# Performance work log

Measured on AMD Instinct MI355X. Metric: run time of the kernel, lower is better.

## Reference

```python
import jax, jax.numpy as jnp
import numpy as np

B = 4
N_TOTAL = 40000
N_SRC0, N_DST0, E0 = 30000, 15000, 360000
N_DST1, E1 = 7500, 180000
D_IN, OUT = 64, 32
H1, C1 = 8, 8
H2, C2 = 1, OUT
NEG_SLOPE = 0.2


def setup_inputs() -> dict:
    key = jax.random.key(0)
    ks = jax.random.split(key, 16)
    inp = {
        'x': jax.random.normal(ks[0], (B, N_TOTAL, D_IN), dtype=jnp.float32),
        'n_id0': jax.random.randint(ks[1], (N_SRC0,), 0, N_SRC0),
        'res_n_id0': jax.random.randint(ks[2], (N_DST0,), 0, N_SRC0),
        'edge_src0': jax.random.randint(ks[3], (E0,), 0, N_SRC0),
        'edge_dst0': jax.random.randint(ks[4], (E0,), 0, N_DST0),
        'res_n_id1': jax.random.randint(ks[5], (N_DST1,), 0, N_DST0),
        'edge_src1': jax.random.randint(ks[6], (E1,), 0, N_DST0),
        'edge_dst1': jax.random.randint(ks[7], (E1,), 0, N_DST1),
        # GATConv params (Glorot-ish scale)
        'W1': jax.random.normal(ks[8], (D_IN, H1 * C1), dtype=jnp.float32) / np.sqrt(D_IN),
        'att_src1': jax.random.normal(ks[9], (H1, C1), dtype=jnp.float32) / np.sqrt(C1),
        'att_dst1': jax.random.normal(ks[10], (H1, C1), dtype=jnp.float32) / np.sqrt(C1),
        'b1': jnp.zeros((H1 * C1,), dtype=jnp.float32),
        'W2': jax.random.normal(ks[11], (H1 * C1, H2 * C2), dtype=jnp.float32) / np.sqrt(H1 * C1),
        'att_src2': jax.random.normal(ks[12], (H2, C2), dtype=jnp.float32) / np.sqrt(C2),
        'att_dst2': jax.random.normal(ks[13], (H2, C2), dtype=jnp.float32) / np.sqrt(C2),
        'b2': jnp.zeros((H2 * C2,), dtype=jnp.float32),
    }
    return inp


def gat_conv(x_src, x_dst, src, dst, W, a_src, a_dst, bias, n_dst, H, C):
    """Bipartite PyG-style GATConv (concat=True, eval mode, no self-loops)."""
    b = x_src.shape[0]
    hs = (x_src @ W).reshape(b, -1, H, C)            # [B, Ns, H, C]
    hd = (x_dst @ W).reshape(b, -1, H, C)            # [B, Nd, H, C]
    es = jnp.einsum('bnhc,hc->bnh', hs, a_src)       # [B, Ns, H]
    ed = jnp.einsum('bnhc,hc->bnh', hd, a_dst)       # [B, Nd, H]
    e = jax.nn.leaky_relu(es[:, src] + ed[:, dst], NEG_SLOPE)  # [B, E, H]
    eT = jnp.swapaxes(e, 0, 1)                       # [E, B, H] (segment over axis 0)
    m = jax.ops.segment_max(eT, dst, num_segments=n_dst)
    p = jnp.exp(eT - m[dst])
    den = jax.ops.segment_sum(p, dst, num_segments=n_dst)
    alpha = p / den[dst]                             # [E, B, H]
    msg = alpha[..., None] * jnp.swapaxes(hs[:, src], 0, 1)    # [E, B, H, C]
    out = jax.ops.segment_sum(msg, dst, num_segments=n_dst)    # [Nd, B, H, C]
    out = jnp.swapaxes(out, 0, 1).reshape(b, n_dst, H * C)
    return out + bias


def reference(x, n_id0, res_n_id0, edge_src0, edge_dst0, res_n_id1, edge_src1,
              edge_dst1, W1, att_src1, att_dst1, b1, W2, att_src2, att_dst2, b2):
    xt = x[:, n_id0, :]                                        # [B, N_SRC0, D_IN]
    h = gat_conv(xt, xt[:, res_n_id0, :], edge_src0, edge_dst0,
                 W1, att_src1, att_dst1, b1, N_DST0, H1, C1)
    h = jax.nn.elu(h)                                          # dropout = identity (eval)
    out = gat_conv(h, h[:, res_n_id1, :], edge_src1, edge_dst1,
                   W2, att_src2, att_dst2, b2, N_DST1, H2, C2)
    return out                                                 # [B, N_DST1, OUT]
```

## Files before the change

### kernel.cpp

```cpp
#include <hip/hip_runtime.h>

#define NB 4
#define NT 40000
#define NS0 30000
#define ND0 15000
#define NE0 360000
#define ND1 7500
#define NE1 180000
#define NEG 0.2f

#define CAP 64
#define K1B ((NB*NS0)/64)
#define SB8 ((NE0 + NE1 + 2047)/2048)

#define BKT(p) ((((p) & 7) << 3) | ((p) >> 3))

typedef __attribute__((ext_vector_type(8))) short bf8;
typedef __attribute__((ext_vector_type(4))) float f4;
typedef __attribute__((ext_vector_type(2))) float f2;

__device__ __forceinline__ unsigned short f2bf(float f) {
    unsigned u = __float_as_uint(f);
    u += 0x7FFF + ((u >> 16) & 1);
    return (unsigned short)(u >> 16);
}
__device__ __forceinline__ f2 upk(unsigned u) {
    f2 r;
    r.x = __uint_as_float(u << 16);
    r.y = __uint_as_float(u & 0xFFFF0000u);
    return r;
}

__global__ __launch_bounds__(256) void kA_gemm_scat(
        const float* __restrict__ x, const int* __restrict__ n_id0,
        const float* __restrict__ W1, const float* __restrict__ a_src,
        const float* __restrict__ a_dst,
        unsigned short* __restrict__ ht1b, float* __restrict__ es1, float* __restrict__ ed1,
        const int* __restrict__ esrc0, const int* __restrict__ edst0,
        const int* __restrict__ esrc1, const int* __restrict__ edst1,
        int* __restrict__ cur0, int* __restrict__ cur1,
        int* __restrict__ srcsort0, int* __restrict__ srcsort1) {
    __shared__ unsigned short xtb[64*72];
    __shared__ unsigned short wtb[64*72];
    __shared__ float asl[64], adl[64];
    if (blockIdx.x >= K1B) {
        int base = (blockIdx.x - K1B) * 2048 + threadIdx.x;
        #pragma unroll
        for (int p = 0; p < 8; ++p) {
            int t = base + p * 256;
            if (t < NE0) {
                int d = edst0[t];
                int pos = atomicAdd(&cur0[d], 1);
                if (pos < CAP) srcsort0[d*CAP + BKT(pos)] = esrc0[t];
            } else if (t < NE0 + NE1) {
                int e = t - NE0;
                int d = edst1[e];
                int pos = atomicAdd(&cur1[d], 1);
                if (pos < CAP) srcsort1[d*CAP + BKT(pos)] = esrc1[e];
            }
        }
        return;
    }
    int bid = blockIdx.x;
    int t = threadIdx.x;
    {
        int k = t >> 2, nb = (t & 3) * 16;
        const float* wrow = &W1[k*64 + nb];
        #pragma unroll
        for (int j = 0; j < 16; j += 4) {
            float4 v = *(const float4*)&wrow[j];
            wtb[(nb+j+0)*72 + k] = f2bf(v.x);
            wtb[(nb+j+1)*72 + k] = f2bf(v.y);
            wtb[(nb+j+2)*72 + k] = f2bf(v.z);
            wtb[(nb+j+3)*72 + k] = f2bf(v.w);
        }
    }
    if (t < 64) { asl[t] = a_src[t]; adl[t] = a_dst[t]; }
    {
        int r   = t >> 2;
        int sub = t & 3;
        int row_s = bid * 64 + r;
        int bs = row_s / NS0;
        int ns = row_s - bs * NS0;
        const float* xrow = x + ((size_t)(bs * NT + n_id0[ns])) * 64;
        #pragma unroll
        for (int j = 0; j < 4; ++j) {
            int kf = (sub + j*4) * 4;
            float4 v = *(const float4*)&xrow[kf];
            ushort4 u;
            u.x = f2bf(v.x); u.y = f2bf(v.y); u.z = f2bf(v.z); u.w = f2bf(v.w);
            *(ushort4*)&xtb[r*72 + kf] = u;
        }
    }
    __syncthreads();
    int w = t >> 6, lane = t & 63, quad = lane >> 4, cl = lane & 15;
    int arow = 16*w + cl;
    bf8 a0 = *(const bf8*)&xtb[arow*72 + quad*8];
    bf8 a1 = *(const bf8*)&xtb[arow*72 + 32 + quad*8];
    f4 acc[4];
    #pragma unroll
    for (int sub = 0; sub < 4; ++sub) {
        int n = sub*16 + cl;
        bf8 b0 = *(const bf8*)&wtb[n*72 + quad*8];
        bf8 b1v = *(const bf8*)&wtb[n*72 + 32 + quad*8];
        f4 c = {0.f, 0.f, 0.f, 0.f};
        c = __builtin_amdgcn_mfma_f32_16x16x32_bf16(a0, b0, c, 0, 0, 0);
        c = __builtin_amdgcn_mfma_f32_16x16x32_bf16(a1, b1v, c, 0, 0, 0);
        acc[sub] = c;
    }
    __syncthreads();
    unsigned short* ob = xtb;
    #pragma unroll
    for (int sub = 0; sub < 4; ++sub)
        #pragma unroll
        for (int r = 0; r < 4; ++r)
            ob[(16*w + 4*quad + r)*64 + sub*16 + cl] = f2bf(acc[sub][r]);
    int rbase = bid*64 + 16*w + quad*4;
    #pragma unroll
    for (int r = 0; r < 4; ++r) {
        #pragma unroll
        for (int sub = 0; sub < 4; ++sub) {
            int col = sub*16 + cl;
            float ps = acc[sub][r] * asl[col];
            float pd = acc[sub][r] * adl[col];
            ps += __shfl_xor(ps, 1); ps += __shfl_xor(ps, 2); ps += __shfl_xor(ps, 4);
            pd += __shfl_xor(pd, 1); pd += __shfl_xor(pd, 2); pd += __shfl_xor(pd, 4);
            if ((cl & 7) == 0) {
                int h = sub*2 + (cl >> 3);
                es1[(rbase + r)*8 + h] = ps;
                ed1[(rbase + r)*8 + h] = pd;
            }
        }
    }
    __syncthreads();
    {
        int row = t >> 3;
        int c8  = t & 7;
        #pragma unroll
        for (int rep = 0; rep < 2; ++rep) {
            int rr2 = row + rep*32;
            uint4 v = *(const uint4*)&ob[rr2*64 + c8*8];
            *(uint4*)&ht1b[((size_t)(bid*64 + rr2))*64 + c8*8] = v;
        }
    }
}

__global__ __launch_bounds__(256) void k3_agg1_node2(
        const int* __restrict__ srcsort0, const int* __restrict__ cur0,
        const int* __restrict__ res0,
        const float* __restrict__ es1, const float* __restrict__ ed1,
        const unsigned short* __restrict__ ht1b, const float* __restrict__ b1,
        const float* __restrict__ W2, const float* __restrict__ a_src2,
        const float* __restrict__ a_dst2,
        float* __restrict__ ht2, float* __restrict__ es2, float* __restrict__ ed2) {
    __shared__ float W2t[32][68];
    __shared__ float as2[32], ad2[32];
    __shared__ float b1l[64];
    __shared__ float hsh[4][64];
    int t = threadIdx.x;
    {
        float4 v0 = *(const float4*)&W2[t*8];
        float4 v1 = *(const float4*)&W2[t*8 + 4];
        int k = t >> 2, c = (t & 3) * 8;
        W2t[c+0][k] = v0.x; W2t[c+1][k] = v0.y; W2t[c+2][k] = v0.z; W2t[c+3][k] = v0.w;
        W2t[c+4][k] = v1.x; W2t[c+5][k] = v1.y; W2t[c+6][k] = v1.z; W2t[c+7][k] = v1.w;
    }
    if (t < 32) { as2[t] = a_src2[t]; ad2[t] = a_dst2[t]; }
    if (t < 64) b1l[t] = b1[t];
    __syncthreads();
    int xcd = blockIdx.x & 7;
    int b = xcd >> 1;
    int chunk = (blockIdx.x >> 3) * 2 + (xcd & 1);
    int wv = t >> 6;
    int d = chunk * 4 + wv;
    int lane = t & 63;
    int grp = lane >> 3;
    int c = lane & 7;
    int dn = res0[d];
    float edv = ed1[(b*NS0 + dn)*8 + c];
    int start = d * CAP;
    int cnt = min(cur0[d], CAP);
    const float* esb = es1 + (size_t)b*NS0*8;
    const unsigned short* htb = ht1b + (size_t)b*NS0*64;
    f2 a01 = {0.f, 0.f}, a23 = {0.f, 0.f}, a45 = {0.f, 0.f}, a67 = {0.f, 0.f};
    float wsum = 0.f;
    int i = grp;
    int pp = start + grp*8;
    int4 sv = *(const int4*)&srcsort0[pp];
    bool v0 = i      < cnt, v1 = i + 8  < cnt,
         v2 = i + 16 < cnt, v3 = i + 24 < cnt;
    int s0 = v0 ? sv.x : 0;
    int s1 = v1 ? sv.y : 0;
    int s2 = v2 ? sv.z : 0;
    int s3 = v3 ? sv.w : 0;
    for (;;) {
        float e0 = esb[s0*8 + c], e1 = esb[s1*8 + c];
        float e2 = esb[s2*8 + c], e3 = esb[s3*8 + c];
        uint4 h0 = *(const uint4*)&htb[(size_t)s0*64 + c*8];
        uint4 h1 = *(const uint4*)&htb[(size_t)s1*64 + c*8];
        uint4 h2 = *(const uint4*)&htb[(size_t)s2*64 + c*8];
        uint4 h3 = *(const uint4*)&htb[(size_t)s3*64 + c*8];
        int ni = i + 32;
        bool nv0 = false, nv1 = false, nv2 = false, nv3 = false;
        int t0 = 0, t1 = 0, t2 = 0, t3 = 0;
        if (ni < cnt) {
            int4 nsv = *(const int4*)&srcsort0[pp + 4];
            nv0 = true;            nv1 = ni + 8  < cnt;
            nv2 = ni + 16 < cnt;   nv3 = ni + 24 < cnt;
            t0 =       nsv.x;
            t1 = nv1 ? nsv.y : 0;
            t2 = nv2 ? nsv.z : 0;
            t3 = nv3 ? nsv.w : 0;
        }
        e0 += edv; e1 += edv; e2 += edv; e3 += edv;
        e0 = e0 > 0.f ? e0 : NEG * e0;
        e1 = e1 > 0.f ? e1 : NEG * e1;
        e2 = e2 > 0.f ? e2 : NEG * e2;
        e3 = e3 > 0.f ? e3 : NEG * e3;
        float w0 = v0 ? __expf(e0) : 0.f;
        float w1 = v1 ? __expf(e1) : 0.f;
        float w2 = v2 ? __expf(e2) : 0.f;
        float w3 = v3 ? __expf(e3) : 0.f;
        a01 += w0 * upk(h0.x); a23 += w0 * upk(h0.y);
        a45 += w0 * upk(h0.z); a67 += w0 * upk(h0.w);
        a01 += w1 * upk(h1.x); a23 += w1 * upk(h1.y);
        a45 += w1 * upk(h1.z); a67 += w1 * upk(h1.w);
        a01 += w2 * upk(h2.x); a23 += w2 * upk(h2.y);
        a45 += w2 * upk(h2.z); a67 += w2 * upk(h2.w);
        a01 += w3 * upk(h3.x); a23 += w3 * upk(h3.y);
        a45 += w3 * upk(h3.z); a67 += w3 * upk(h3.w);
        wsum += (w0 + w1) + (w2 + w3);
        i = ni; pp += 4;
        s0 = t0; s1 = t1; s2 = t2; s3 = t3;
        v0 = nv0; v1 = nv1; v2 = nv2; v3 = nv3;
        if (i >= cnt) break;
    }
    float acc[8] = {a01.x, a01.y, a23.x, a23.y, a45.x, a45.y, a67.x, a67.y};
    int g0 = grp & 1, g1 = (grp >> 1) & 1, g2 = grp >> 2;
    float n0, n1, n2, n3;
    {
        float s, r;
        s = g0 ? acc[0] : acc[1]; r = __shfl_xor(s, 8);  n0 = (g0 ? acc[1] : acc[0]) + r;
        s = g0 ? acc[2] : acc[3]; r = __shfl_xor(s, 8);  n1 = (g0 ? acc[3] : acc[2]) + r;
        s = g0 ? acc[4] : acc[5]; r = __shfl_xor(s, 8);  n2 = (g0 ? acc[5] : acc[4]) + r;
        s = g0 ? acc[6] : acc[7]; r = __shfl_xor(s, 8);  n3 = (g0 ? acc[7] : acc[6]) + r;
    }
    float m0, m1;
    {
        float s, r;
        s = g1 ? n0 : n1; r = __shfl_xor(s, 16); m0 = (g1 ? n1 : n0) + r;
        s = g1 ? n2 : n3; r = __shfl_xor(s, 16); m1 = (g1 ? n3 : n2) + r;
    }
    float fin;
    {
        float s = g2 ? m0 : m1; float r = __shfl_xor(s, 32); fin = (g2 ? m1 : m0) + r;
    }
    wsum += __shfl_xor(wsum, 8); wsum += __shfl_xor(wsum, 16); wsum += __shfl_xor(wsum, 32);
    float inv = cnt > 0 ? 1.f / wsum : 0.f;
    float o = fin * inv + b1l[(c << 3) | grp];
    o = o > 0.f ? o : __expf(o) - 1.f;
    hsh[wv][(c << 3) | grp] = o;
    int c2 = lane & 31, half = lane >> 5;
    const float4* hp = (const float4*)&hsh[wv][half * 32];
    const float4* wp = (const float4*)&W2t[c2][half * 32];
    float acc2 = 0.f;
    #pragma unroll
    for (int q = 0; q < 8; ++q) {
        float4 hv = hp[q];
        float4 w4 = wp[q];
        acc2 = fmaf(hv.x, w4.x, acc2); acc2 = fmaf(hv.y, w4.y, acc2);
        acc2 = fmaf(hv.z, w4.z, acc2); acc2 = fmaf(hv.w, w4.w, acc2);
    }
    acc2 += __shfl_xor(acc2, 32);
    float ps = acc2 * as2[c2];
    float pd = acc2 * ad2[c2];
    ps += __shfl_xor(ps, 1); ps += __shfl_xor(ps, 2); ps += __shfl_xor(ps, 4);
    ps += __shfl_xor(ps, 8); ps += __shfl_xor(ps, 16);
    pd += __shfl_xor(pd, 1); pd += __shfl_xor(pd, 2); pd += __shfl_xor(pd, 4);
    pd += __shfl_xor(pd, 8); pd += __shfl_xor(pd, 16);
    int row = b*ND0 + d;
    if (half == 0) ht2[(size_t)row*32 + c2] = acc2;
    if (lane == 0) { es2[row] = ps; ed2[row] = pd; }
}

__global__ __launch_bounds__(256) void k7_agg2(
        const int* __restrict__ srcsort1, const int* __restrict__ cur1,
        const int* __restrict__ res1,
        const float* __restrict__ es2, const float* __restrict__ ed2,
        const float* __restrict__ ht2, const float* __restrict__ b2,
        float* __restrict__ outp) {
    int xcd = blockIdx.x & 7;
    int b = xcd >> 1;
    int chunk = (blockIdx.x >> 3) * 2 + (xcd & 1);
    if (chunk >= ND1/4) return;
    int d = chunk * 4 + (threadIdx.x >> 6);
    int lane = threadIdx.x & 63;
    int grp = lane >> 3;
    int c = lane & 7;
    int dn = res1[d];
    float edv = ed2[b*ND0 + dn];
    int start = d * CAP;
    int cnt = min(cur1[d], CAP);
    const float* esb = es2 + (size_t)b*ND0;
    const float* htb = ht2 + (size_t)b*ND0*32;
    f4 accv = {0.f, 0.f, 0.f, 0.f};
    float wsum = 0.f;
    int i = grp;
    int pp = start + grp*8;
    int4 sv = *(const int4*)&srcsort1[pp];
    bool v0 = i      < cnt, v1 = i + 8  < cnt,
         v2 = i + 16 < cnt, v3 = i + 24 < cnt;
    int s0 = v0 ? sv.x : 0;
    int s1 = v1 ? sv.y : 0;
    int s2 = v2 ? sv.z : 0;
    int s3 = v3 ? sv.w : 0;
    for (;;) {
        float lg0 = esb[s0], lg1 = esb[s1], lg2 = esb[s2], lg3 = esb[s3];
        f4 h0 = *(const f4*)&htb[(size_t)s0*32 + c*4];
        f4 h1 = *(const f4*)&htb[(size_t)s1*32 + c*4];
        f4 h2 = *(const f4*)&htb[(size_t)s2*32 + c*4];
        f4 h3 = *(const f4*)&htb[(size_t)s3*32 + c*4];
        int ni = i + 32;
        bool nv0 = false, nv1 = false, nv2 = false, nv3 = false;
        int t0 = 0, t1 = 0, t2 = 0, t3 = 0;
        if (ni < cnt) {
            int4 nsv = *(const int4*)&srcsort1[pp + 4];
            nv0 = true;            nv1 = ni + 8  < cnt;
            nv2 = ni + 16 < cnt;   nv3 = ni + 24 < cnt;
            t0 =       nsv.x;
            t1 = nv1 ? nsv.y : 0;
            t2 = nv2 ? nsv.z : 0;
            t3 = nv3 ? nsv.w : 0;
        }
        lg0 += edv; lg1 += edv; lg2 += edv; lg3 += edv;
        lg0 = lg0 > 0.f ? lg0 : NEG * lg0;
        lg1 = lg1 > 0.f ? lg1 : NEG * lg1;
        lg2 = lg2 > 0.f ? lg2 : NEG * lg2;
        lg3 = lg3 > 0.f ? lg3 : NEG * lg3;
        float w0 = v0 ? __expf(lg0) : 0.f;
        float w1 = v1 ? __expf(lg1) : 0.f;
        float w2 = v2 ? __expf(lg2) : 0.f;
        float w3 = v3 ? __expf(lg3) : 0.f;
        accv += w0 * h0;
        accv += w1 * h1;
        accv += w2 * h2;
        accv += w3 * h3;
        wsum += (w0 + w1) + (w2 + w3);
        i = ni; pp += 4;
        s0 = t0; s1 = t1; s2 = t2; s3 = t3;
        v0 = nv0; v1 = nv1; v2 = nv2; v3 = nv3;
        if (i >= cnt) break;
    }
    float ax = accv.x, ay = accv.y, az = accv.z, aw = accv.w;
    ax += __shfl_xor(ax, 8); ax += __shfl_xor(ax, 16); ax += __shfl_xor(ax, 32);
    ay += __shfl_xor(ay, 8); ay += __shfl_xor(ay, 16); ay += __shfl_xor(ay, 32);
    az += __shfl_xor(az, 8); az += __shfl_xor(az, 16); az += __shfl_xor(az, 32);
    aw += __shfl_xor(aw, 8); aw += __shfl_xor(aw, 16); aw += __shfl_xor(aw, 32);
    wsum += __shfl_xor(wsum, 8); wsum += __shfl_xor(wsum, 16); wsum += __shfl_xor(wsum, 32);
    if (grp == 0) {
        float inv = cnt > 0 ? 1.f / wsum : 0.f;
        float4 bb = *(const float4*)&b2[c*4];
        float4 o;
        o.x = ax*inv + bb.x; o.y = ay*inv + bb.y;
        o.z = az*inv + bb.z; o.w = aw*inv + bb.w;
        *(float4*)&outp[((size_t)(b*ND1 + d))*32 + c*4] = o;
    }
}

extern "C" void kernel_launch(void* const* d_in, const int* in_sizes, int n_in,
                              void* d_out, int out_size, void* d_ws, size_t ws_size,
                              hipStream_t stream) {
    const float* x        = (const float*)d_in[0];
    const int*   n_id0    = (const int*)d_in[1];
    const int*   res0     = (const int*)d_in[2];
    const int*   esrc0    = (const int*)d_in[3];
    const int*   edst0    = (const int*)d_in[4];
    const int*   res1     = (const int*)d_in[5];
    const int*   esrc1    = (const int*)d_in[6];
    const int*   edst1    = (const int*)d_in[7];
    const float* W1       = (const float*)d_in[8];
    const float* a_src1   = (const float*)d_in[9];
    const float* a_dst1   = (const float*)d_in[10];
    const float* b1       = (const float*)d_in[11];
    const float* W2       = (const float*)d_in[12];
    const float* a_src2   = (const float*)d_in[13];
    const float* a_dst2   = (const float*)d_in[14];
    const float* b2       = (const float*)d_in[15];
    float* outp = (float*)d_out;

    char* base = (char*)d_ws;
    unsigned short* ht1b = (unsigned short*)base;
    float* es1  = (float*)(base + 15360000);
    float* ed1  = es1 + 960000;
    float* ht2  = ed1 + 960000;
    float* es2  = ht2 + 1920000;
    float* ed2  = es2 + 60000;
    int* cur0     = (int*)(ed2 + 60000);
    int* cur1     = cur0 + ND0;
    int* srcsort0 = cur1 + ND1;
    int* srcsort1 = srcsort0 + ND0*CAP;

    hipMemsetAsync(cur0, 0, (ND0 + ND1) * sizeof(int), stream);
    kA_gemm_scat<<<K1B + SB8, 256, 0, stream>>>(x, n_id0, W1, a_src1, a_dst1,
                                                ht1b, es1, ed1,
                                                esrc0, edst0, esrc1, edst1,
                                                cur0, cur1, srcsort0, srcsort1);
    k3_agg1_node2<<<NB*(ND0/4), 256, 0, stream>>>(srcsort0, cur0, res0, es1, ed1, ht1b, b1,
                                                  W2, a_src2, a_dst2, ht2, es2, ed2);
    k7_agg2<<<7504, 256, 0, stream>>>(srcsort1, cur1, res1, es2, ed2, ht2, b2, outp);
}
```

Before: 184.1 us.

## Interleave scatter blocks with GEMM blocks and process two row tiles per block

```diff
diff --git a/kernel.cpp b/kernel.cpp
--- a/kernel.cpp
+++ b/kernel.cpp
@@ -10,8 +10,8 @@
 #define NEG 0.2f
 
 #define CAP 64
-#define K1B ((NB*NS0)/64)
-#define SB8 ((NE0 + NE1 + 2047)/2048)
+#define GEMB 938
+#define SBI  264
 
 #define BKT(p) ((((p) & 7) << 3) | ((p) >> 3))
 
@@ -43,8 +43,16 @@
     __shared__ unsigned short xtb[64*72];
     __shared__ unsigned short wtb[64*72];
     __shared__ float asl[64], adl[64];
-    if (blockIdx.x >= K1B) {
-        int base = (blockIdx.x - K1B) * 2048 + threadIdx.x;
+    int bid = blockIdx.x;
+    int sid = -1, gid = 0;
+    if (bid < SBI*4) {
+        if ((bid & 3) == 0) sid = bid >> 2;
+        else gid = (bid >> 2) * 3 + (bid & 3) - 1;
+    } else {
+        gid = bid - SBI;
+    }
+    if (sid >= 0) {
+        int base = sid * 2048 + threadIdx.x;
         #pragma unroll
         for (int p = 0; p < 8; ++p) {
             int t = base + p * 256;
@@ -61,7 +69,6 @@
         }
         return;
     }
-    int bid = blockIdx.x;
     int t = threadIdx.x;
     {
         int k = t >> 2, nb = (t & 3) * 16;
@@ -76,72 +83,80 @@
         }
     }
     if (t < 64) { asl[t] = a_src[t]; adl[t] = a_dst[t]; }
-    {
-        int r   = t >> 2;
-        int sub = t & 3;
-        int row_s = bid * 64 + r;
-        int bs = row_s / NS0;
-        int ns = row_s - bs * NS0;
-        const float* xrow = x + ((size_t)(bs * NT + n_id0[ns])) * 64;
-        #pragma unroll
-        for (int j = 0; j < 4; ++j) {
-            int kf = (sub + j*4) * 4;
-            float4 v = *(const float4*)&xrow[kf];
-            ushort4 u;
-            u.x = f2bf(v.x); u.y = f2bf(v.y); u.z = f2bf(v.z); u.w = f2bf(v.w);
-            *(ushort4*)&xtb[r*72 + kf] = u;
-        }
-    }
-    __syncthreads();
-    int w = t >> 6, lane = t & 63, quad = lane >> 4, cl = lane & 15;
-    int arow = 16*w + cl;
-    bf8 a0 = *(const bf8*)&xtb[arow*72 + quad*8];
-    bf8 a1 = *(const bf8*)&xtb[arow*72 + 32 + quad*8];
-    f4 acc[4];
-    #pragma unroll
-    for (int sub = 0; sub < 4; ++sub) {
-        int n = sub*16 + cl;
-        bf8 b0 = *(const bf8*)&wtb[n*72 + quad*8];
-        bf8 b1v = *(const bf8*)&wtb[n*72 + 32 + quad*8];
-        f4 c = {0.f, 0.f, 0.f, 0.f};
-        c = __builtin_amdgcn_mfma_f32_16x16x32_bf16(a0, b0, c, 0, 0, 0);
-        c = __builtin_amdgcn_mfma_f32_16x16x32_bf16(a1, b1v, c, 0, 0, 0);
-        acc[sub] = c;
-    }
-    __syncthreads();
-    unsigned short* ob = xtb;
-    #pragma unroll
-    for (int sub = 0; sub < 4; ++sub)
-        #pragma unroll
-        for (int r = 0; r < 4; ++r)
-            ob[(16*w + 4*quad + r)*64 + sub*16 + cl] = f2bf(acc[sub][r]);
-    int rbase = bid*64 + 16*w + quad*4;
-    #pragma unroll
-    for (int r = 0; r < 4; ++r) {
+    for (int tile = 0; tile < 2; ++tile) {
+        int rowbase = gid * 128 + tile * 64;
+        {
+            int r   = t >> 2;
+            int sub = t & 3;
+            int row_s = rowbase + r;
+            int rs = row_s < NB*NS0 ? row_s : 0;
+            int bs = rs / NS0;
+            int ns = rs - bs * NS0;
+            const float* xrow = x + ((size_t)(bs * NT + n_id0[ns])) * 64;
+            #pragma unroll
+            for (int j = 0; j < 4; ++j) {
+                int kf = (sub + j*4) * 4;
+                float4 v = *(const float4*)&xrow[kf];
+                ushort4 u;
+                u.x = f2bf(v.x); u.y = f2bf(v.y); u.z = f2bf(v.z); u.w = f2bf(v.w);
+                *(ushort4*)&xtb[r*72 + kf] = u;
+            }
+        }
+        __syncthreads();
+        int w = t >> 6, lane = t & 63, quad = lane >> 4, cl = lane & 15;
+        int arow = 16*w + cl;
+        bf8 a0 = *(const bf8*)&xtb[arow*72 + quad*8];
+        bf8 a1 = *(const bf8*)&xtb[arow*72 + 32 + quad*8];
+        f4 acc[4];
         #pragma unroll
         for (int sub = 0; sub < 4; ++sub) {
-            int col = sub*16 + cl;
-            float ps = acc[sub][r] * asl[col];
-            float pd = acc[sub][r] * adl[col];
-            ps += __shfl_xor(ps, 1); ps += __shfl_xor(ps, 2); ps += __shfl_xor(ps, 4);
-            pd += __shfl_xor(pd, 1); pd += __shfl_xor(pd, 2); pd += __shfl_xor(pd, 4);
-            if ((cl & 7) == 0) {
-                int h = sub*2 + (cl >> 3);
-                es1[(rbase + r)*8 + h] = ps;
-                ed1[(rbase + r)*8 + h] = pd;
+            int n = sub*16 + cl;
+            bf8 b0 = *(const bf8*)&wtb[n*72 + quad*8];
+            bf8 b1v = *(const bf8*)&wtb[n*72 + 32 + quad*8];
+            f4 c = {0.f, 0.f, 0.f, 0.f};
+            c = __builtin_amdgcn_mfma_f32_16x16x32_bf16(a0, b0, c, 0, 0, 0);
+            c = __builtin_amdgcn_mfma_f32_16x16x32_bf16(a1, b1v, c, 0, 0, 0);
+            acc[sub] = c;
+        }
+        __syncthreads();
+        unsigned short* ob = xtb;
+        #pragma unroll
+        for (int sub = 0; sub < 4; ++sub)
+            #pragma unroll
+            for (int r = 0; r < 4; ++r)
+                ob[(16*w + 4*quad + r)*64 + sub*16 + cl] = f2bf(acc[sub][r]);
+        int rbase = rowbase + 16*w + quad*4;
+        #pragma unroll
+        for (int r = 0; r < 4; ++r) {
+            #pragma unroll
+            for (int sub = 0; sub < 4; ++sub) {
+                int col = sub*16 + cl;
+                float ps = acc[sub][r] * asl[col];
+                float pd = acc[sub][r] * adl[col];
+                ps += __shfl_xor(ps, 1); ps += __shfl_xor(ps, 2); ps += __shfl_xor(ps, 4);
+                pd += __shfl_xor(pd, 1); pd += __shfl_xor(pd, 2); pd += __shfl_xor(pd, 4);
+                if ((cl & 7) == 0 && rbase + r < NB*NS0) {
+                    int h = sub*2 + (cl >> 3);
+                    es1[(rbase + r)*8 + h] = ps;
+                    ed1[(rbase + r)*8 + h] = pd;
+                }
             }
         }
-    }
-    __syncthreads();
-    {
-        int row = t >> 3;
-        int c8  = t & 7;
-        #pragma unroll
-        for (int rep = 0; rep < 2; ++rep) {
-            int rr2 = row + rep*32;
-            uint4 v = *(const uint4*)&ob[rr2*64 + c8*8];
-            *(uint4*)&ht1b[((size_t)(bid*64 + rr2))*64 + c8*8] = v;
-        }
+        __syncthreads();
+        {
+            int row = t >> 3;
+            int c8  = t & 7;
+            #pragma unroll
+            for (int rep = 0; rep < 2; ++rep) {
+                int rr2 = row + rep*32;
+                int grow = rowbase + rr2;
+                if (grow < NB*NS0) {
+                    uint4 v = *(const uint4*)&ob[rr2*64 + c8*8];
+                    *(uint4*)&ht1b[(size_t)grow*64 + c8*8] = v;
+                }
+            }
+        }
+        __syncthreads();
     }
 }
 
@@ -401,7 +416,7 @@
     int* srcsort1 = srcsort0 + ND0*CAP;
 
     hipMemsetAsync(cur0, 0, (ND0 + ND1) * sizeof(int), stream);
-    kA_gemm_scat<<<K1B + SB8, 256, 0, stream>>>(x, n_id0, W1, a_src1, a_dst1,
+    kA_gemm_scat<<<SBI*4 + (GEMB - SBI*3), 256, 0, stream>>>(x, n_id0, W1, a_src1, a_dst1,
                                                 ht1b, es1, ed1,
                                                 esrc0, edst0, esrc1, edst1,
                                                 cur0, cur1, srcsort0, srcsort1);
```

Measured after the change: 190.9 us. 1.04x slower.
